# Kernel optimization log

Measured on AMD Instinct MI355X. Metric: run time of the kernel, lower is better.

## Reference

```python
import jax, jax.numpy as jnp
import numpy as np

DMODEL = 128
HEAD = 128
SEQ = 4096
BATCH = 16

def setup_inputs() -> dict:
    key = jax.random.key(0)
    kx, kq, kk, kv = jax.random.split(key, 4)
    x = jax.random.normal(kx, (BATCH, SEQ, DMODEL), dtype=jnp.float32)
    # nn.Linear(dmodel, head_size, bias=False): store as (dmodel, head_size) so q = x @ Wq
    s = 1.0 / np.sqrt(DMODEL)
    Wq = jax.random.uniform(kq, (DMODEL, HEAD), jnp.float32, -s, s)
    Wk = jax.random.uniform(kk, (DMODEL, HEAD), jnp.float32, -s, s)
    Wv = jax.random.uniform(kv, (DMODEL, HEAD), jnp.float32, -s, s)
    return {"x": x, "Wq": Wq, "Wk": Wk, "Wv": Wv}

def reference(x, Wq, Wk, Wv):
    B, L, _ = x.shape
    scale = HEAD ** (-0.5)
    q = jnp.einsum('bld,dh->blh', x, Wq)
    k = jnp.einsum('bld,dh->blh', x, Wk)
    v = jnp.einsum('bld,dh->blh', x, Wv)
    wei = jnp.einsum('bqh,bkh->bqk', q, k) * scale  # (B, L, L)
    causal = jnp.tril(jnp.ones((L, L), dtype=bool))
    wei = jnp.where(causal, wei, -jnp.inf)
    wei = jax.nn.softmax(wei, axis=-1)
    y = jnp.einsum('bqk,bkh->bqh', wei, v)
    return y
```

## Files before the change

kernel.cpp:

```cpp
#include <hip/hip_runtime.h>
#include <hip/hip_bf16.h>
#include <stdint.h>

#define SEQ   4096
#define DM    128
#define KVB   128

typedef __attribute__((ext_vector_type(8)))  short  bf16x8;
typedef __attribute__((ext_vector_type(16))) float  f32x16;

#define SCALE_LOG2E 0.12751743f

__device__ __forceinline__ f32x16 mfma_32x32x16(bf16x8 a, bf16x8 b, f32x16 c) {
  return __builtin_amdgcn_mfma_f32_32x32x16_bf16(a, b, c, 0, 0, 0);
}

__device__ __forceinline__ void gload16(const void* g, void* l) {
  __builtin_amdgcn_global_load_lds(
      (const __attribute__((address_space(1))) unsigned int*)g,
      (__attribute__((address_space(3))) unsigned int*)l, 16, 0, 0);
}

__device__ __forceinline__ unsigned pack2bf(float a, float b) {
  float2 t; t.x = a; t.y = b;
  __hip_bfloat162 h = __float22bfloat162_rn(t);
  union { __hip_bfloat162 h2; unsigned u; } cv;
  cv.h2 = h;
  return cv.u;
}

__device__ __forceinline__ float us2f(unsigned short u) {
  union { unsigned int i; float f; } c; c.i = ((unsigned)u) << 16; return c.f;
}

__device__ __forceinline__ float fast_exp2(float x) {
#if defined(__has_builtin)
#if __has_builtin(__builtin_amdgcn_exp2f)
  return __builtin_amdgcn_exp2f(x);
#else
  return exp2f(x);
#endif
#else
  return exp2f(x);
#endif
}

#define SBAR() __builtin_amdgcn_sched_barrier(0)

__global__ void prep_w(const float* __restrict__ Wq, const float* __restrict__ Wk,
                       const float* __restrict__ Wv, __hip_bfloat16* __restrict__ Wb) {
  int t = blockIdx.x * 256 + threadIdx.x;
  if (t >= 12 * 8 * 64) return;
  int ct  = t >> 9;
  int rem = t & 511;
  int s   = rem >> 6;
  int l   = rem & 63;
  const float* W = (ct < 4) ? Wq : (ct < 8) ? Wk : Wv;
  float c = (ct < 4) ? SCALE_LOG2E : 1.0f;
  int h  = (ct & 3) * 32 + (l & 31);
  int d0 = 16 * s + 8 * (l >> 5);
  union { __hip_bfloat16 h8[8]; bf16x8 v; } u;
#pragma unroll
  for (int i = 0; i < 8; ++i) u.h8[i] = __float2bfloat16(W[(d0 + i) * DM + h] * c);
  *(bf16x8*)&Wb[(size_t)t * 8] = u.v;
}

__global__ void __launch_bounds__(256, 2)
proj(const float* __restrict__ x, const __hip_bfloat16* __restrict__ Wb,
     __hip_bfloat16* __restrict__ qw, __hip_bfloat16* __restrict__ kw,
     __hip_bfloat16* __restrict__ vtw) {
  __shared__ __hip_bfloat16 slab[4][1024];
  const int wave = threadIdx.x >> 6, lane = threadIdx.x & 63;
  const int l31 = lane & 31, hi = lane >> 5;
  const int t0 = blockIdx.x * 128 + wave * 32;
  const int trow = t0 + l31;

  bf16x8 af[8];
#pragma unroll
  for (int s = 0; s < 8; ++s) {
    const float* px = x + (size_t)trow * DM + 16 * s + 8 * hi;
    float4 u0 = *(const float4*)px;
    float4 u1 = *(const float4*)(px + 4);
    union { bf16x8 v; unsigned u[4]; } fr;
    fr.u[0] = pack2bf(u0.x, u0.y);
    fr.u[1] = pack2bf(u0.z, u0.w);
    fr.u[2] = pack2bf(u1.x, u1.y);
    fr.u[3] = pack2bf(u1.z, u1.w);
    af[s] = fr.v;
  }

  for (int ct = 0; ct < 12; ++ct) {
    f32x16 acc;
#pragma unroll
    for (int j = 0; j < 16; ++j) acc[j] = 0.f;
#pragma unroll
    for (int s = 0; s < 8; ++s) {
      bf16x8 bfr = *(const bf16x8*)&Wb[(size_t)((ct * 8 + s) * 64 + lane) * 8];
      acc = mfma_32x32x16(af[s], bfr, acc);
    }
    __syncthreads();
#pragma unroll
    for (int j = 0; j < 16; ++j) {
      int r = (j & 3) + 8 * (j >> 2) + 4 * hi;
      slab[wave][r * 32 + l31] = __float2bfloat16(acc[j]);
    }
    __syncthreads();
    if (ct < 8) {
      __hip_bfloat16* dst = (ct < 4) ? qw : kw;
      int hb = (ct & 3) * 32;
#pragma unroll
      for (int p = 0; p < 2; ++p) {
        int eidx = p * 512 + lane * 8;
        int tr = eidx >> 5, c = eidx & 31;
        *(bf16x8*)&dst[(size_t)(t0 + tr) * DM + hb + c] =
            *(const bf16x8*)&slab[wave][eidx];
      }
    } else {
      int d  = lane >> 1;
      int th = (lane & 1) * 16;
      int dg = (ct & 3) * 32 + d;
      int bb = t0 >> 12;
      int tl = t0 & 4095;
      __hip_bfloat16* dst = vtw + ((size_t)bb * DM + dg) * SEQ + tl + th;
#pragma unroll
      for (int k = 0; k < 4; ++k) {
        union { unsigned short u4[4]; uint2 v; } pkv;
#pragma unroll
        for (int e = 0; e < 4; ++e) {
          union { __hip_bfloat16 hh; unsigned short us; } cv;
          cv.hh = slab[wave][(th + 4 * k + e) * 32 + d];
          pkv.u4[e] = cv.us;
        }
        *(uint2*)&dst[4 * k] = pkv.v;
      }
    }
  }
}

__device__ __forceinline__ void stage_k(const char* kb, int tile, char* kdst,
                                        int tid) {
  const char* ksrc = kb + (size_t)tile * (KVB * 256);
#pragma unroll
  for (int p = 0; p < 4; ++p) {
    int lin = p * 8192 + tid * 16;
    int row = lin >> 8, cb = lin & 255;
    int col = cb ^ ((row & 15) << 4);
    gload16(ksrc + row * 256 + col, kdst + lin);
  }
}

__device__ __forceinline__ void stage_v(const char* vb, int tile, char* vdst,
                                        int tid) {
  const char* vsrc = vb + (size_t)tile * (KVB * 2);
#pragma unroll
  for (int p = 0; p < 4; ++p) {
    int lin = p * 8192 + tid * 16;
    int row = lin >> 8, cb = lin & 255;
    int col = cb ^ ((row & 15) << 4);
    gload16(vsrc + (size_t)row * 8192 + col, vdst + lin);
  }
}

__global__ void __launch_bounds__(512)
attn(const __hip_bfloat16* __restrict__ qw, const __hip_bfloat16* __restrict__ kw,
     const __hip_bfloat16* __restrict__ vtw, float* __restrict__ out,
     float* __restrict__ lsumA, float* __restrict__ lsumB,
     __hip_bfloat16* __restrict__ partB) {
  __shared__ __align__(16) char lds[131072];
  const int bid = blockIdx.x;
  const int xcd = bid & 7;
  const int g   = bid >> 3;
  const int b   = xcd + 8 * (g & 1);
  const int j16 = g >> 1;
  const int i   = j16 & 7;
  const int isB = j16 >> 3;
  const int bigQ = 15 - i;
  const int m = b * 8 + i;

  const int wave = threadIdx.x >> 6, lane = threadIdx.x & 63;
  const int l31 = lane & 31, hi = lane >> 5;
  const int tid = threadIdx.x;

  const char* kb = (const char*)(kw + (size_t)b * SEQ * DM);
  const char* vb = (const char*)(vtw + (size_t)b * DM * SEQ);

  char* k_cur = lds;         char* k_nxt = lds + 32768;
  char* v_cur = lds + 65536; char* v_nxt = lds + 98304;

  auto visit = [&](int qt, int t0, int cnt, int mode) {
    const int q0 = qt << 8;
    const int qrow = q0 + wave * 32 + l31;
    const int qminw = q0 + wave * 32;
    const int qmaxw = qminw + 31;

    bf16x8 qf[8];
    {
      const __hip_bfloat16* qb = qw + ((size_t)b * SEQ + qrow) * DM;
#pragma unroll
      for (int ss = 0; ss < 8; ++ss) qf[ss] = *(const bf16x8*)&qb[16 * ss + 8 * hi];
    }
    f32x16 yacc[4];
#pragma unroll
    for (int dt = 0; dt < 4; ++dt)
#pragma unroll
      for (int jj = 0; jj < 16; ++jj) yacc[dt][jj] = 0.f;
    f32x16 psum;
#pragma unroll
    for (int jj = 0; jj < 16; ++jj) psum[jj] = 0.f;

    stage_k(kb, t0, k_cur, tid);
    stage_v(vb, t0, v_cur, tid);
    SBAR();
    asm volatile("s_waitcnt vmcnt(0)" ::: "memory");
    __builtin_amdgcn_s_barrier();
    SBAR();

    for (int u = 0; u < cnt; ++u) {
      const int t  = t0 + u;
      const int un = (u + 1 < cnt) ? u + 1 : u;
      stage_k(kb, t0 + un, k_nxt, tid);
      stage_v(vb, t0 + un, v_nxt, tid);

#pragma unroll
      for (int h = 0; h < 2; ++h) {
        const int kv0 = t * KVB + 64 * h;
        if (kv0 > qmaxw) continue;
        f32x16 sa, sb;
#pragma unroll
        for (int jj = 0; jj < 16; ++jj) { sa[jj] = 0.f; sb[jj] = 0.f; }
        __builtin_amdgcn_s_setprio(1);
#pragma unroll
        for (int ss = 0; ss < 8; ++ss) {
          int cbs = 32 * ss + 16 * hi;
          int r0 = 64 * h + l31, r1 = 64 * h + l31 + 32;
          bf16x8 k0 = *(const bf16x8*)&k_cur[r0 * 256 + (cbs ^ ((r0 & 15) << 4))];
          bf16x8 k1 = *(const bf16x8*)&k_cur[r1 * 256 + (cbs ^ ((r1 & 15) << 4))];
          sa = mfma_32x32x16(k0, qf[ss], sa);
          sb = mfma_32x32x16(k1, qf[ss], sb);
        }
        __builtin_amdgcn_s_setprio(0);
        if (kv0 + 63 > qminw) {
#pragma unroll
          for (int jj = 0; jj < 16; ++jj) {
            int rr = (jj & 3) + 8 * (jj >> 2) + 4 * hi;
            sa[jj] = (kv0 + rr      > qrow) ? -1e30f : sa[jj];
            sb[jj] = (kv0 + 32 + rr > qrow) ? -1e30f : sb[jj];
          }
        }
#pragma unroll
        for (int jj = 0; jj < 16; ++jj) sa[jj] = fast_exp2(sa[jj]);
#pragma unroll
        for (int jj = 0; jj < 16; ++jj) sb[jj] = fast_exp2(sb[jj]);
#pragma unroll
        for (int jj = 0; jj < 16; ++jj) psum[jj] += sa[jj] + sb[jj];

#pragma unroll
        for (int a = 0; a < 2; ++a) {
          unsigned pk[8];
#pragma unroll
          for (int jj = 0; jj < 8; ++jj) {
            float lo  = a ? sb[2 * jj]     : sa[2 * jj];
            float hi2 = a ? sb[2 * jj + 1] : sa[2 * jj + 1];
            pk[jj] = pack2bf(lo, hi2);
          }
#pragma unroll
          for (int s2 = 0; s2 < 2; ++s2) {
            int base = 4 * s2;
            unsigned a0 = pk[base + 0], b0 = pk[base + 2];
            unsigned a1 = pk[base + 1], b1 = pk[base + 3];
            asm volatile("v_permlane32_swap_b32 %0, %1" : "+v"(a0), "+v"(b0));
            asm volatile("v_permlane32_swap_b32 %0, %1" : "+v"(a1), "+v"(b1));
            union { bf16x8 v; unsigned u[4]; } pf;
            pf.u[0] = a0;
            pf.u[1] = a1;
            pf.u[2] = b0;
            pf.u[3] = b1;
            __builtin_amdgcn_s_setprio(1);
#pragma unroll
            for (int dt = 0; dt < 4; ++dt) {
              int vrow = 32 * dt + l31;
              int vcol = 128 * h + 64 * a + 32 * s2 + 16 * hi;
              bf16x8 vf = *(const bf16x8*)&v_cur[vrow * 256 +
                                                 (vcol ^ ((vrow & 15) << 4))];
              yacc[dt] = mfma_32x32x16(vf, pf.v, yacc[dt]);
            }
            __builtin_amdgcn_s_setprio(0);
          }
        }
      }
      SBAR();
      asm volatile("s_waitcnt vmcnt(0)" ::: "memory");
      __builtin_amdgcn_s_barrier();
      SBAR();
      char* tmp = k_cur; k_cur = k_nxt; k_nxt = tmp;
      tmp = v_cur; v_cur = v_nxt; v_nxt = tmp;
    }

    float lsum = 0.f;
#pragma unroll
    for (int jj = 0; jj < 16; ++jj) lsum += psum[jj];
    lsum += __shfl_xor(lsum, 32);

    float* ob = out + ((size_t)b * SEQ + qrow) * DM;
    const int row = wave * 32 + l31;
    if (mode == 0) {
      float inv = 1.0f / lsum;
#pragma unroll
      for (int dt = 0; dt < 4; ++dt) {
#pragma unroll
        for (int g2 = 0; g2 < 4; ++g2) {
          float4 v;
          v.x = yacc[dt][4 * g2 + 0] * inv;
          v.y = yacc[dt][4 * g2 + 1] * inv;
          v.z = yacc[dt][4 * g2 + 2] * inv;
          v.w = yacc[dt][4 * g2 + 3] * inv;
          *(float4*)&ob[32 * dt + 8 * g2 + 4 * hi] = v;
        }
      }
    } else if (mode == 1) {
#pragma unroll
      for (int dt = 0; dt < 4; ++dt) {
#pragma unroll
        for (int g2 = 0; g2 < 4; ++g2) {
          float4 v;
          v.x = yacc[dt][4 * g2 + 0];
          v.y = yacc[dt][4 * g2 + 1];
          v.z = yacc[dt][4 * g2 + 2];
          v.w = yacc[dt][4 * g2 + 3];
          *(float4*)&ob[32 * dt + 8 * g2 + 4 * hi] = v;
        }
      }
      if (hi == 0) lsumA[m * 256 + row] = lsum;
    } else {
      __hip_bfloat16* pb = partB + ((size_t)m * 256 + row) * DM;
#pragma unroll
      for (int dt = 0; dt < 4; ++dt) {
#pragma unroll
        for (int g2 = 0; g2 < 4; ++g2) {
          uint2 pv;
          pv.x = pack2bf(yacc[dt][4 * g2 + 0], yacc[dt][4 * g2 + 1]);
          pv.y = pack2bf(yacc[dt][4 * g2 + 2], yacc[dt][4 * g2 + 3]);
          *(uint2*)&pb[32 * dt + 8 * g2 + 4 * hi] = pv;
        }
      }
      if (hi == 0) lsumB[m * 256 + row] = lsum;
    }
  };

  if (!isB) {
    visit(bigQ, 0, 17, 1);
  } else {
    visit(bigQ, 17, 15 - 2 * i, 2);
    visit(i, 0, 2 * i + 2, 0);
  }
}

__global__ void __launch_bounds__(256)
merge(float* __restrict__ out, const float* __restrict__ lsumA,
      const float* __restrict__ lsumB, const __hip_bfloat16* __restrict__ partB) {
  __shared__ float invls[256];
  const int m = blockIdx.x;
  const int b = m >> 3;
  const int Q = 15 - (m & 7);
  const int tid = threadIdx.x;
  invls[tid] = 1.0f / (lsumA[m * 256 + tid] + lsumB[m * 256 + tid]);
  __syncthreads();
  float4* o4 = (float4*)(out + ((size_t)b * SEQ + (size_t)Q * 256) * DM);
  const __hip_bfloat16* pb = partB + (size_t)m * 256 * DM;
#pragma unroll
  for (int k = 0; k < 32; ++k) {
    int e4 = tid + 256 * k;
    int row = e4 >> 5;
    float4 a = o4[e4];
    union { uint2 v; unsigned short s[4]; } pv;
    pv.v = *(const uint2*)&pb[e4 * 4];
    float inv = invls[row];
    float4 r;
    r.x = (a.x + us2f(pv.s[0])) * inv;
    r.y = (a.y + us2f(pv.s[1])) * inv;
    r.z = (a.z + us2f(pv.s[2])) * inv;
    r.w = (a.w + us2f(pv.s[3])) * inv;
    o4[e4] = r;
  }
}

extern "C" void kernel_launch(void* const* d_in, const int* in_sizes, int n_in,
                              void* d_out, int out_size, void* d_ws, size_t ws_size,
                              hipStream_t stream) {
  const float* x  = (const float*)d_in[0];
  const float* Wq = (const float*)d_in[1];
  const float* Wk = (const float*)d_in[2];
  const float* Wv = (const float*)d_in[3];
  float* out = (float*)d_out;

  char* ws = (char*)d_ws;
  __hip_bfloat16* qw    = (__hip_bfloat16*)(ws);
  __hip_bfloat16* kw    = (__hip_bfloat16*)(ws + (size_t)16 * 1024 * 1024);
  __hip_bfloat16* vtw   = (__hip_bfloat16*)(ws + (size_t)32 * 1024 * 1024);
  char* base48 = ws + (size_t)48 * 1024 * 1024;
  __hip_bfloat16* Wb    = (__hip_bfloat16*)(base48);
  float*          lsumA = (float*)(base48 + (size_t)1 * 1024 * 1024);
  float*          lsumB = (float*)(base48 + (size_t)2 * 1024 * 1024);
  __hip_bfloat16* partB = (__hip_bfloat16*)(base48 + (size_t)3 * 1024 * 1024);

  prep_w<<<24, 256, 0, stream>>>(Wq, Wk, Wv, Wb);
  proj<<<512, 256, 0, stream>>>(x, Wb, qw, kw, vtw);
  attn<<<256, 512, 0, stream>>>(qw, kw, vtw, out, lsumA, lsumB, partB);
  merge<<<128, 256, 0, stream>>>(out, lsumA, lsumB, partB);
}
```

Before: 120.2 us.

## Halve KV tile and stagger wave groups to overlap QK with softmax-PV

```diff
diff --git a/kernel.cpp b/kernel.cpp
--- a/kernel.cpp
+++ b/kernel.cpp
@@ -4,7 +4,7 @@
 
 #define SEQ   4096
 #define DM    128
-#define KVB   128
+#define KVB   64
 
 typedef __attribute__((ext_vector_type(8)))  short  bf16x8;
 typedef __attribute__((ext_vector_type(16))) float  f32x16;
@@ -141,7 +141,7 @@
                                         int tid) {
   const char* ksrc = kb + (size_t)tile * (KVB * 256);
 #pragma unroll
-  for (int p = 0; p < 4; ++p) {
+  for (int p = 0; p < 2; ++p) {
     int lin = p * 8192 + tid * 16;
     int row = lin >> 8, cb = lin & 255;
     int col = cb ^ ((row & 15) << 4);
@@ -153,11 +153,12 @@
                                         int tid) {
   const char* vsrc = vb + (size_t)tile * (KVB * 2);
 #pragma unroll
-  for (int p = 0; p < 4; ++p) {
+  for (int p = 0; p < 2; ++p) {
     int lin = p * 8192 + tid * 16;
     int row = lin >> 8, cb = lin & 255;
     int col = cb ^ ((row & 15) << 4);
-    gload16(vsrc + (size_t)row * 8192 + col, vdst + lin);
+    size_t so = (size_t)(2 * row + (col >> 7)) * 8192 + (size_t)(col & 127);
+    gload16(vsrc + so, vdst + lin);
   }
 }
 
@@ -166,7 +167,7 @@
      const __hip_bfloat16* __restrict__ vtw, float* __restrict__ out,
      float* __restrict__ lsumA, float* __restrict__ lsumB,
      __hip_bfloat16* __restrict__ partB) {
-  __shared__ __align__(16) char lds[131072];
+  __shared__ __align__(16) char lds[81920];
   const int bid = blockIdx.x;
   const int xcd = bid & 7;
   const int g   = bid >> 3;
@@ -180,18 +181,23 @@
   const int wave = threadIdx.x >> 6, lane = threadIdx.x & 63;
   const int l31 = lane & 31, hi = lane >> 5;
   const int tid = threadIdx.x;
+  const bool grpB = wave >= 4;
 
   const char* kb = (const char*)(kw + (size_t)b * SEQ * DM);
   const char* vb = (const char*)(vtw + (size_t)b * DM * SEQ);
 
-  char* k_cur = lds;         char* k_nxt = lds + 32768;
-  char* v_cur = lds + 65536; char* v_nxt = lds + 98304;
+  char* kbuf0 = lds;
+  char* kbuf1 = lds + 16384;
+  char* vbuf0 = lds + 32768;
+  char* vbuf1 = lds + 49152;
+  char* vbuf2 = lds + 65536;
 
   auto visit = [&](int qt, int t0, int cnt, int mode) {
     const int q0 = qt << 8;
     const int qrow = q0 + wave * 32 + l31;
     const int qminw = q0 + wave * 32;
     const int qmaxw = qminw + 31;
+    const int tlast = t0 + cnt - 1;
 
     bf16x8 qf[8];
     {
@@ -208,93 +214,117 @@
 #pragma unroll
     for (int jj = 0; jj < 16; ++jj) psum[jj] = 0.f;
 
-    stage_k(kb, t0, k_cur, tid);
-    stage_v(vb, t0, v_cur, tid);
+    auto QK = [&](const char* k_use, f32x16& Sa, f32x16& Sb) {
+#pragma unroll
+      for (int jj = 0; jj < 16; ++jj) { Sa[jj] = 0.f; Sb[jj] = 0.f; }
+      __builtin_amdgcn_s_setprio(1);
+#pragma unroll
+      for (int ss = 0; ss < 8; ++ss) {
+        int cbs = 32 * ss + 16 * hi;
+        int r0 = l31, r1 = l31 + 32;
+        bf16x8 k0 = *(const bf16x8*)&k_use[r0 * 256 + (cbs ^ ((r0 & 15) << 4))];
+        bf16x8 k1 = *(const bf16x8*)&k_use[r1 * 256 + (cbs ^ ((r1 & 15) << 4))];
+        Sa = mfma_32x32x16(k0, qf[ss], Sa);
+        Sb = mfma_32x32x16(k1, qf[ss], Sb);
+      }
+      __builtin_amdgcn_s_setprio(0);
+    };
+
+    auto SMPV = [&](int kv0, const char* v_use, f32x16& Sa, f32x16& Sb) {
+      if (kv0 + 63 > qminw) {
+#pragma unroll
+        for (int jj = 0; jj < 16; ++jj) {
+          int rr = (jj & 3) + 8 * (jj >> 2) + 4 * hi;
+          Sa[jj] = (kv0 + rr      > qrow) ? -1e30f : Sa[jj];
+          Sb[jj] = (kv0 + 32 + rr > qrow) ? -1e30f : Sb[jj];
+        }
+      }
+#pragma unroll
+      for (int jj = 0; jj < 16; ++jj) Sa[jj] = fast_exp2(Sa[jj]);
+#pragma unroll
+      for (int jj = 0; jj < 16; ++jj) Sb[jj] = fast_exp2(Sb[jj]);
+#pragma unroll
+      for (int jj = 0; jj < 16; ++jj) psum[jj] += Sa[jj] + Sb[jj];
+#pragma unroll
+      for (int a = 0; a < 2; ++a) {
+        unsigned pk[8];
+#pragma unroll
+        for (int jj = 0; jj < 8; ++jj) {
+          float lo  = a ? Sb[2 * jj]     : Sa[2 * jj];
+          float hi2 = a ? Sb[2 * jj + 1] : Sa[2 * jj + 1];
+          pk[jj] = pack2bf(lo, hi2);
+        }
+#pragma unroll
+        for (int s2 = 0; s2 < 2; ++s2) {
+          int base = 4 * s2;
+          unsigned a0 = pk[base + 0], b0 = pk[base + 2];
+          unsigned a1 = pk[base + 1], b1 = pk[base + 3];
+          asm volatile("v_permlane32_swap_b32 %0, %1" : "+v"(a0), "+v"(b0));
+          asm volatile("v_permlane32_swap_b32 %0, %1" : "+v"(a1), "+v"(b1));
+          union { bf16x8 v; unsigned u[4]; } pf;
+          pf.u[0] = a0;
+          pf.u[1] = a1;
+          pf.u[2] = b0;
+          pf.u[3] = b1;
+          __builtin_amdgcn_s_setprio(1);
+#pragma unroll
+          for (int dt = 0; dt < 4; ++dt) {
+            int vrow = (l31 >> 1) + 16 * dt;
+            int vcol = (l31 & 1) * 128 + 64 * a + 32 * s2 + 16 * hi;
+            bf16x8 vf = *(const bf16x8*)&v_use[vrow * 256 +
+                                               (vcol ^ ((vrow & 15) << 4))];
+            yacc[dt] = mfma_32x32x16(vf, pf.v, yacc[dt]);
+          }
+          __builtin_amdgcn_s_setprio(0);
+        }
+      }
+    };
+
+    stage_k(kb, t0, kbuf0, tid);
+    stage_v(vb, t0, vbuf0, tid);
     SBAR();
     asm volatile("s_waitcnt vmcnt(0)" ::: "memory");
     __builtin_amdgcn_s_barrier();
     SBAR();
 
+    f32x16 sa, sb;
+    int vs = 1, vc = 0, vp = 2;
+    char* vptr[3] = {vbuf0, vbuf1, vbuf2};
+
     for (int u = 0; u < cnt; ++u) {
       const int t  = t0 + u;
-      const int un = (u + 1 < cnt) ? u + 1 : u;
-      stage_k(kb, t0 + un, k_nxt, tid);
-      stage_v(vb, t0 + un, v_nxt, tid);
-
-#pragma unroll
-      for (int h = 0; h < 2; ++h) {
-        const int kv0 = t * KVB + 64 * h;
-        if (kv0 > qmaxw) continue;
-        f32x16 sa, sb;
-#pragma unroll
-        for (int jj = 0; jj < 16; ++jj) { sa[jj] = 0.f; sb[jj] = 0.f; }
-        __builtin_amdgcn_s_setprio(1);
-#pragma unroll
-        for (int ss = 0; ss < 8; ++ss) {
-          int cbs = 32 * ss + 16 * hi;
-          int r0 = 64 * h + l31, r1 = 64 * h + l31 + 32;
-          bf16x8 k0 = *(const bf16x8*)&k_cur[r0 * 256 + (cbs ^ ((r0 & 15) << 4))];
-          bf16x8 k1 = *(const bf16x8*)&k_cur[r1 * 256 + (cbs ^ ((r1 & 15) << 4))];
-          sa = mfma_32x32x16(k0, qf[ss], sa);
-          sb = mfma_32x32x16(k1, qf[ss], sb);
-        }
-        __builtin_amdgcn_s_setprio(0);
-        if (kv0 + 63 > qminw) {
-#pragma unroll
-          for (int jj = 0; jj < 16; ++jj) {
-            int rr = (jj & 3) + 8 * (jj >> 2) + 4 * hi;
-            sa[jj] = (kv0 + rr      > qrow) ? -1e30f : sa[jj];
-            sb[jj] = (kv0 + 32 + rr > qrow) ? -1e30f : sb[jj];
-          }
-        }
-#pragma unroll
-        for (int jj = 0; jj < 16; ++jj) sa[jj] = fast_exp2(sa[jj]);
-#pragma unroll
-        for (int jj = 0; jj < 16; ++jj) sb[jj] = fast_exp2(sb[jj]);
-#pragma unroll
-        for (int jj = 0; jj < 16; ++jj) psum[jj] += sa[jj] + sb[jj];
-
-#pragma unroll
-        for (int a = 0; a < 2; ++a) {
-          unsigned pk[8];
-#pragma unroll
-          for (int jj = 0; jj < 8; ++jj) {
-            float lo  = a ? sb[2 * jj]     : sa[2 * jj];
-            float hi2 = a ? sb[2 * jj + 1] : sa[2 * jj + 1];
-            pk[jj] = pack2bf(lo, hi2);
-          }
-#pragma unroll
-          for (int s2 = 0; s2 < 2; ++s2) {
-            int base = 4 * s2;
-            unsigned a0 = pk[base + 0], b0 = pk[base + 2];
-            unsigned a1 = pk[base + 1], b1 = pk[base + 3];
-            asm volatile("v_permlane32_swap_b32 %0, %1" : "+v"(a0), "+v"(b0));
-            asm volatile("v_permlane32_swap_b32 %0, %1" : "+v"(a1), "+v"(b1));
-            union { bf16x8 v; unsigned u[4]; } pf;
-            pf.u[0] = a0;
-            pf.u[1] = a1;
-            pf.u[2] = b0;
-            pf.u[3] = b1;
-            __builtin_amdgcn_s_setprio(1);
-#pragma unroll
-            for (int dt = 0; dt < 4; ++dt) {
-              int vrow = 32 * dt + l31;
-              int vcol = 128 * h + 64 * a + 32 * s2 + 16 * hi;
-              bf16x8 vf = *(const bf16x8*)&v_cur[vrow * 256 +
-                                                 (vcol ^ ((vrow & 15) << 4))];
-              yacc[dt] = mfma_32x32x16(vf, pf.v, yacc[dt]);
-            }
-            __builtin_amdgcn_s_setprio(0);
-          }
-        }
+      const int tn = (u + 1 < cnt) ? t + 1 : tlast;
+      char* k_cur = (u & 1) ? kbuf1 : kbuf0;
+      char* k_nxt = (u & 1) ? kbuf0 : kbuf1;
+      stage_k(kb, tn, k_nxt, tid);
+      stage_v(vb, tn, vptr[vs], tid);
+
+      const int kv0 = t * KVB;
+      if (!grpB) {
+        if (kv0 <= qmaxw) {
+          QK(k_cur, sa, sb);
+          SMPV(kv0, vptr[vc], sa, sb);
+        }
+      } else {
+        if (u > 0) {
+          const int kv0p = (t - 1) * KVB;
+          if (kv0p <= qmaxw) SMPV(kv0p, vptr[vp], sa, sb);
+        }
+        if (kv0 <= qmaxw) QK(k_cur, sa, sb);
       }
       SBAR();
       asm volatile("s_waitcnt vmcnt(0)" ::: "memory");
       __builtin_amdgcn_s_barrier();
       SBAR();
-      char* tmp = k_cur; k_cur = k_nxt; k_nxt = tmp;
-      tmp = v_cur; v_cur = v_nxt; v_nxt = tmp;
-    }
+      int t3 = vp; vp = vc; vc = vs; vs = t3;
+    }
+    if (grpB) {
+      const int kv0l = tlast * KVB;
+      if (kv0l <= qmaxw) SMPV(kv0l, vptr[vp], sa, sb);
+    }
+    SBAR();
+    __builtin_amdgcn_s_barrier();
+    SBAR();
 
     float lsum = 0.f;
 #pragma unroll
@@ -348,10 +378,10 @@
   };
 
   if (!isB) {
-    visit(bigQ, 0, 17, 1);
+    visit(bigQ, 0, 34, 1);
   } else {
-    visit(bigQ, 17, 15 - 2 * i, 2);
-    visit(i, 0, 2 * i + 2, 0);
+    visit(bigQ, 34, 30 - 4 * i, 2);
+    visit(i, 0, 4 * i + 4, 0);
   }
 }
 
```

Measured after the change: 133.9 us. 11.4% more time.
